# Kernel tuning notes

Measured on AMD Instinct MI355X. Metric: run time of the kernel, lower is better.

The kernel has to match this reference:

```python
import jax, jax.numpy as jnp
import numpy as np

B, LQ, LK, E, H = 4, 2048, 2048, 768, 12
D = E // H  # head_dim = 64
SCALE = 0.25 / np.sqrt(D)
LN_EPS = 1e-5


def _layernorm(x, g, b):
    mu = jnp.mean(x, axis=-1, keepdims=True)
    var = jnp.mean(jnp.square(x - mu), axis=-1, keepdims=True)
    return (x - mu) * jax.lax.rsqrt(var + LN_EPS) * g + b


def _rope(x, f):
    # x: [B,H,L,D]; f: [L,D//2,2] (real, imag) -- complex multiply on interleaved pairs
    xr = x.reshape(*x.shape[:-1], D // 2, 2)
    fr = f[None, None]  # [1,1,L,D//2,2]
    real = xr[..., 0] * fr[..., 0] - xr[..., 1] * fr[..., 1]
    imag = xr[..., 0] * fr[..., 1] + xr[..., 1] * fr[..., 0]
    return jnp.stack([real, imag], axis=-1).reshape(x.shape)


def setup_inputs() -> dict:
    key = jax.random.key(0)
    ks = jax.random.split(key, 8)
    x_q = jax.random.normal(ks[0], (B, LQ, E), jnp.float32)
    x_kv = jax.random.normal(ks[1], (B, LK, E), jnp.float32)
    # unit-magnitude rotary tables (cos, sin of random angles)
    ang_q = jax.random.uniform(ks[2], (LQ, D // 2), jnp.float32, 0.0, 2 * np.pi)
    ang_k = jax.random.uniform(ks[3], (LK, D // 2), jnp.float32, 0.0, 2 * np.pi)
    freqs_cis = jnp.stack([jnp.cos(ang_q), jnp.sin(ang_q)], axis=-1)
    freqs_cis_cross = jnp.stack([jnp.cos(ang_k), jnp.sin(ang_k)], axis=-1)
    Wq = jax.random.normal(ks[4], (E, E), jnp.float32) * 0.02
    Wkv = jax.random.normal(ks[5], (E, 2 * E), jnp.float32) * 0.02
    Wo = jax.random.normal(ks[6], (E, E), jnp.float32) * 0.02
    bo = jnp.zeros((E,), jnp.float32)
    return {
        'x_q': x_q, 'x_kv': x_kv,
        'freqs_cis': freqs_cis, 'freqs_cis_cross': freqs_cis_cross,
        'Wq': Wq, 'Wkv': Wkv, 'Wo': Wo, 'bo': bo,
        'ln_q_g': jnp.ones((E,), jnp.float32), 'ln_q_b': jnp.zeros((E,), jnp.float32),
        'ln_kv_g': jnp.ones((E,), jnp.float32), 'ln_kv_b': jnp.zeros((E,), jnp.float32),
        'gain': jnp.array(1.0, jnp.float32),
    }


def reference(x_q, x_kv, freqs_cis, freqs_cis_cross, Wq, Wkv, Wo, bo,
              ln_q_g, ln_q_b, ln_kv_g, ln_kv_b, gain):
    q = _layernorm(x_q, ln_q_g, ln_q_b) @ Wq                 # [B,LQ,E]
    kv = _layernorm(x_kv, ln_kv_g, ln_kv_b) @ Wkv            # [B,LK,2E]
    k, v = jnp.split(kv, 2, axis=-1)
    # b l (h d) -> b h l d
    q = q.reshape(B, LQ, H, D).transpose(0, 2, 1, 3)
    k = k.reshape(B, LK, H, D).transpose(0, 2, 1, 3)
    v = v.reshape(B, LK, H, D).transpose(0, 2, 1, 3)
    q = _rope(q, freqs_cis)
    k = _rope(k, freqs_cis_cross)
    attn = jnp.einsum('bhqd,bhkd->bhqk', q, k) * SCALE       # full O(L^2) matrix
    attn = jax.nn.softmax(attn, axis=-1)
    out = jnp.einsum('bhqk,bhkd->bhqd', attn, v)
    out = out.transpose(0, 2, 1, 3).reshape(B, LQ, E)        # b h l d -> b l (h d)
    return gain * (out @ Wo + bo)
```

## Files before the change

### kernel.cpp

```cpp
#include <hip/hip_runtime.h>
#include <hip/hip_bf16.h>

#define B_ 4
#define LQ_ 2048
#define LK_ 2048
#define E_ 768
#define H_ 12
#define D_ 64
#define SCALE_ 0.03125f
#define QSCALE_ 0.04508422f

using short8 = __attribute__((ext_vector_type(8))) short;
using f32x4  = __attribute__((ext_vector_type(4))) float;
using f32x16 = __attribute__((ext_vector_type(16))) float;

__device__ inline unsigned short f2bf(float f) {
    union { float f; unsigned u; } v; v.f = f;
    unsigned r = (v.u + 0x7FFFu + ((v.u >> 16) & 1u)) >> 16;
    return (unsigned short)r;
}

__device__ inline unsigned pkbf(float a, float b) {
    union { float f; unsigned u; } x, y; x.f = a; y.f = b;
    return ((x.u + 0x8000u) >> 16) | ((y.u + 0x8000u) & 0xffff0000u);
}

__device__ inline unsigned pkcvt(float a, float b) {
    float2 p; p.x = a; p.y = b;
    __hip_bfloat162 pb = __float22bfloat162_rn(p);
    union { __hip_bfloat162 h; unsigned u; } c; c.h = pb;
    return c.u;
}

__device__ inline void gll16(const void* g, void* l) {
    __builtin_amdgcn_global_load_lds(
        (const __attribute__((address_space(1))) unsigned int*)g,
        (__attribute__((address_space(3))) unsigned int*)l, 16, 0, 0);
}

__global__ __launch_bounds__(256) void ln_kernel(
    const float* __restrict__ xq, const float* __restrict__ xkv,
    const float* __restrict__ gq, const float* __restrict__ bq,
    const float* __restrict__ gk, const float* __restrict__ bk,
    unsigned short* __restrict__ yq, unsigned short* __restrict__ ykv)
{
    int wave = threadIdx.x >> 6, lane = threadIdx.x & 63;
    int row = blockIdx.x * 4 + wave;
    const float* x; const float* g; const float* be; unsigned short* y;
    if (row < 8192) { x = xq; g = gq; be = bq; y = yq; }
    else { row -= 8192; x = xkv; g = gk; be = bk; y = ykv; }
    const float* xr = x + (size_t)row * E_;
    float4 v[3];
    float s = 0.f;
#pragma unroll
    for (int i = 0; i < 3; i++) {
        v[i] = *(const float4*)(xr + i * 256 + lane * 4);
        s += v[i].x + v[i].y + v[i].z + v[i].w;
    }
#pragma unroll
    for (int off = 32; off >= 1; off >>= 1) s += __shfl_xor(s, off);
    float mu = s * (1.0f / E_);
    float q = 0.f;
#pragma unroll
    for (int i = 0; i < 3; i++) {
        float dx = v[i].x - mu, dy = v[i].y - mu, dz = v[i].z - mu, dw = v[i].w - mu;
        q += dx * dx + dy * dy + dz * dz + dw * dw;
    }
#pragma unroll
    for (int off = 32; off >= 1; off >>= 1) q += __shfl_xor(q, off);
    float rstd = rsqrtf(q * (1.0f / E_) + 1e-5f);
    unsigned short* yr = y + (size_t)row * E_;
#pragma unroll
    for (int i = 0; i < 3; i++) {
        int c = i * 256 + lane * 4;
        float4 gv = *(const float4*)(g + c);
        float4 bv = *(const float4*)(be + c);
        ushort4 o;
        o.x = f2bf((v[i].x - mu) * rstd * gv.x + bv.x);
        o.y = f2bf((v[i].y - mu) * rstd * gv.y + bv.y);
        o.z = f2bf((v[i].z - mu) * rstd * gv.z + bv.z);
        o.w = f2bf((v[i].w - mu) * rstd * gv.w + bv.w);
        *(ushort4*)(yr + c) = o;
    }
}

__global__ __launch_bounds__(256) void transpose3_kernel(
    const float* __restrict__ Wq, const float* __restrict__ Wkv, const float* __restrict__ Wo,
    unsigned short* __restrict__ WqT, unsigned short* __restrict__ WkvT, unsigned short* __restrict__ WoT)
{
    __shared__ float tile[32][33];
    int z = blockIdx.z;
    const float* in; unsigned short* out; int C;
    if (z == 0)      { in = Wq;  out = WqT;  C = E_; }
    else if (z == 1) { in = Wkv; out = WkvT; C = 2 * E_; }
    else             { in = Wo;  out = WoT;  C = E_; }
    int c0 = blockIdx.x * 32, r0 = blockIdx.y * 32;
    if (c0 >= C) return;
    int tx = threadIdx.x & 31, ty = threadIdx.x >> 5;
#pragma unroll
    for (int i = 0; i < 32; i += 8)
        tile[ty + i][tx] = in[(size_t)(r0 + ty + i) * C + c0 + tx];
    __syncthreads();
#pragma unroll
    for (int i = 0; i < 32; i += 8)
        out[(size_t)(c0 + ty + i) * E_ + r0 + tx] = f2bf(tile[tx][ty + i]);
}

#define BN 128
#define BK 64
template<int BMT>
__global__ __launch_bounds__(256) void gemm_kernel(
    const unsigned short* __restrict__ A, const unsigned short* __restrict__ Bt,
    int K, int mode,
    unsigned short* __restrict__ outQ, const float* __restrict__ freqs,
    unsigned short* __restrict__ outK, unsigned short* __restrict__ outV,
    float* __restrict__ outF, const float* __restrict__ bo, const float* __restrict__ gain)
{
    constexpr int MT = (BMT == 128) ? 4 : 2;
    constexpr int SMEMN = (BMT == 128) ? 128 * 136 : (BMT * 64 + 128 * 64);
    __shared__ __align__(16) unsigned short smem[SMEMN];
    auto Asm = (unsigned short (*)[BK])smem;
    auto Bsm = (unsigned short (*)[BK])(smem + BMT * BK);

    int tid = threadIdx.x;
    int wave = tid >> 6, lane = tid & 63;
    int quad = lane >> 4, l16 = lane & 15;
    int waveM = (wave >> 1) * (MT * 16), waveN = (wave & 1) * 64;
    int bm = blockIdx.x * BMT, bn = blockIdx.y * BN;
    int ro = lane >> 3, cx = lane & 7;
    int sco = ((cx ^ ro) * 8);

    f32x4 acc[MT][4] = {};

    for (int k0 = 0; k0 < K; k0 += BK) {
        const unsigned short* Ag = A + (size_t)(bm + wave * (BMT / 4) + ro) * K + k0 + sco;
        const unsigned short* Bg = Bt + (size_t)(bn + wave * 32 + ro) * K + k0 + sco;
#pragma unroll
        for (int i = 0; i < BMT / 32; i++)
            gll16(Ag + (size_t)(i * 8) * K, &Asm[wave * (BMT / 4) + i * 8][0]);
#pragma unroll
        for (int i = 0; i < 4; i++)
            gll16(Bg + (size_t)(i * 8) * K, &Bsm[wave * 32 + i * 8][0]);
        __syncthreads();
#pragma unroll
        for (int kk = 0; kk < BK; kk += 32) {
            short8 fa[MT], fb[4];
#pragma unroll
            for (int t = 0; t < 4; t++) {
                int pos = ((quad + (kk >> 3)) ^ (l16 & 7)) * 8;
                if (t < MT) fa[t] = *(const short8*)(&Asm[waveM + t * 16 + l16][pos]);
                fb[t] = *(const short8*)(&Bsm[waveN + t * 16 + l16][pos]);
            }
#pragma unroll
            for (int mt = 0; mt < MT; mt++)
#pragma unroll
                for (int nt = 0; nt < 4; nt++)
                    acc[mt][nt] = __builtin_amdgcn_mfma_f32_16x16x32_bf16(fa[mt], fb[nt], acc[mt][nt], 0, 0, 0);
        }
        __syncthreads();
    }

    if (BMT == 128 && mode == 1 && bn >= E_) {
        auto T = (unsigned short (*)[136])smem;
#pragma unroll
        for (int mt = 0; mt < MT; mt++) {
#pragma unroll
            for (int nt = 0; nt < 4; nt++) {
                int ml = waveM + mt * 16 + quad * 4;
                int nl = waveN + nt * 16 + l16;
                *(unsigned*)&T[nl][ml]     = pkbf(acc[mt][nt][0], acc[mt][nt][1]);
                *(unsigned*)&T[nl][ml + 2] = pkbf(acc[mt][nt][2], acc[mt][nt][3]);
            }
        }
        __syncthreads();
        int nnbase = bn - E_;
        int bb = bm >> 11, l0 = bm & (LQ_ - 1);
#pragma unroll
        for (int it = 0; it < 8; it++) {
            int row = it * 16 + (tid >> 4);
            int hh = (nnbase + row) >> 6, dd = (nnbase + row) & 63;
            short8 v = *(const short8*)&T[row][(tid & 15) * 8];
            *(short8*)(outV + (((size_t)bb * H_ + hh) * D_ + dd) * LK_ + l0 + (tid & 15) * 8) = v;
        }
        return;
    }

    float gg = (mode == 2) ? gain[0] : 0.f;
#pragma unroll
    for (int mt = 0; mt < MT; mt++) {
#pragma unroll
        for (int nt = 0; nt < 4; nt++) {
#pragma unroll
            for (int r = 0; r < 4; r++) {
                int m = bm + waveM + mt * 16 + quad * 4 + r;
                int n = bn + waveN + nt * 16 + l16;
                float v = acc[mt][nt][r];
                if (mode == 2) {
                    outF[(size_t)m * E_ + n] = gg * (v + bo[n]);
                } else {
                    int l = m & (LQ_ - 1), bb = m >> 11;
                    float partner = __shfl_xor(v, 1);
                    int h = n >> 6, dd = n & 63;
                    const float* f = freqs + ((size_t)l * 32 + (dd >> 1)) * 2;
                    float f0 = f[0], f1 = f[1];
                    float o = ((dd & 1) == 0) ? (v * f0 - partner * f1)
                                              : (partner * f1 + v * f0);
                    if (mode == 0) o *= QSCALE_;
                    unsigned short* dst = (mode == 0) ? outQ : outK;
                    dst[(((size_t)bb * H_ + h) * LQ_ + l) * D_ + dd] = f2bf(o);
                }
            }
        }
    }
}

__global__ __launch_bounds__(256) void attn_kernel(
    const unsigned short* __restrict__ Qg, const unsigned short* __restrict__ Kg,
    const unsigned short* __restrict__ Vt, unsigned short* __restrict__ O)
{
    __shared__ unsigned short Ksm[2][64][64];
    __shared__ unsigned short Vsm[2][64][64];

    int tid = threadIdx.x;
    int wave = tid >> 6, lane = tid & 63;
    int l32 = lane & 31, hi = lane >> 5;
    int bh = blockIdx.x;
    int b = bh / H_, h = bh % H_;
    int qbase = blockIdx.y * 128 + wave * 32;

    const size_t head = (size_t)bh * LK_ * D_;
    const unsigned short* Qh = Qg + head;
    const unsigned short* Kh = Kg + head;
    const unsigned short* Vh = Vt + head;

    short8 qf[4];
#pragma unroll
    for (int dc = 0; dc < 4; dc++)
        qf[dc] = *(const short8*)(Qh + (size_t)(qbase + l32) * D_ + dc * 16 + hi * 8);

    f32x16 oacc[2] = {};
    float lsum = 0.f;

    int ro = lane >> 3, cx = lane & 7;
    int sco = ((cx ^ ro) * 8);
    int sw = l32 & 7;

    {
        const unsigned short* Kp = Kh + (size_t)(wave * 16 + ro) * D_ + sco;
        const unsigned short* Vp = Vh + (size_t)(wave * 16 + ro) * LK_ + sco;
        gll16(Kp,            &Ksm[0][wave * 16][0]);
        gll16(Kp + 8 * D_,   &Ksm[0][wave * 16 + 8][0]);
        gll16(Vp,            &Vsm[0][wave * 16][0]);
        gll16(Vp + 8 * LK_,  &Vsm[0][wave * 16 + 8][0]);
    }
    asm volatile("s_waitcnt vmcnt(0)" ::: "memory");

    int buf = 0;
    for (int kt = 0; kt < LK_; kt += 64, buf ^= 1) {
        if (kt + 64 < LK_) {
            const unsigned short* Kp = Kh + (size_t)(kt + 64 + wave * 16 + ro) * D_ + sco;
            const unsigned short* Vp = Vh + (size_t)(wave * 16 + ro) * LK_ + kt + 64 + sco;
            gll16(Kp,           &Ksm[buf ^ 1][wave * 16][0]);
            gll16(Kp + 8 * D_,  &Ksm[buf ^ 1][wave * 16 + 8][0]);
            gll16(Vp,           &Vsm[buf ^ 1][wave * 16][0]);
            gll16(Vp + 8 * LK_, &Vsm[buf ^ 1][wave * 16 + 8][0]);
            asm volatile("s_waitcnt vmcnt(4)\ns_barrier" ::: "memory");
        } else {
            asm volatile("s_waitcnt vmcnt(0)\ns_barrier" ::: "memory");
        }

#pragma unroll
        for (int half = 0; half < 2; half++) {
            f32x16 st = {};
#pragma unroll
            for (int dc = 0; dc < 4; dc++) {
                int pos = ((dc * 2 + hi) ^ sw) * 8;
                short8 kfr = *(const short8*)(&Ksm[buf][half * 32 + l32][pos]);
                st = __builtin_amdgcn_mfma_f32_32x32x16_bf16(kfr, qf[dc], st, 0, 0, 0);
            }
            unsigned pks[8];
#pragma unroll
            for (int t = 0; t < 8; t++) {
                float p0 = __builtin_amdgcn_exp2f(st[2 * t]);
                float p1 = __builtin_amdgcn_exp2f(st[2 * t + 1]);
                lsum += p0 + p1;
                pks[t] = pkcvt(p0, p1);
            }
            unsigned y[8];
#pragma unroll
            for (int t = 0; t < 8; t++) y[t] = (unsigned)__shfl_xor((int)pks[t], 32);

#pragma unroll
            for (int kk = 0; kk < 2; kk++) {
                union { unsigned u[4]; short8 s; } pf;
#pragma unroll
                for (int g = 0; g < 4; g++) {
                    int t0 = kk * 4 + (g & 1);
                    unsigned own = hi ? pks[t0 + 2] : pks[t0];
                    unsigned oth = hi ? y[t0 + 2]   : y[t0];
                    pf.u[g] = ((g >> 1) == hi) ? own : oth;
                }
#pragma unroll
                for (int dt = 0; dt < 2; dt++) {
                    int pos = (((half * 2 + kk) * 2 + hi) ^ sw) * 8;
                    short8 vfr = *(const short8*)(&Vsm[buf][dt * 32 + l32][pos]);
                    oacc[dt] = __builtin_amdgcn_mfma_f32_32x32x16_bf16(pf.s, vfr, oacc[dt], 0, 0, 0);
                }
            }
        }
        asm volatile("s_waitcnt lgkmcnt(0)\ns_barrier" ::: "memory");
    }

    lsum += __shfl_xor(lsum, 32);
    float inv = 1.f / lsum;
#pragma unroll
    for (int reg = 0; reg < 16; reg++) {
        int ql = (reg & 3) + 8 * (reg >> 2) + 4 * hi;
        float iq = __shfl(inv, ql);
        int q = qbase + ql;
        size_t base = ((size_t)b * LQ_ + q) * E_ + h * D_;
#pragma unroll
        for (int dt = 0; dt < 2; dt++)
            O[base + dt * 32 + l32] = f2bf(oacc[dt][reg] * iq);
    }
}

extern "C" void kernel_launch(void* const* d_in, const int* in_sizes, int n_in,
                              void* d_out, int out_size, void* d_ws, size_t ws_size,
                              hipStream_t stream)
{
    const float* x_q     = (const float*)d_in[0];
    const float* x_kv    = (const float*)d_in[1];
    const float* freqs_q = (const float*)d_in[2];
    const float* freqs_k = (const float*)d_in[3];
    const float* Wq      = (const float*)d_in[4];
    const float* Wkv     = (const float*)d_in[5];
    const float* Wo      = (const float*)d_in[6];
    const float* bo      = (const float*)d_in[7];
    const float* ln_q_g  = (const float*)d_in[8];
    const float* ln_q_b  = (const float*)d_in[9];
    const float* ln_kv_g = (const float*)d_in[10];
    const float* ln_kv_b = (const float*)d_in[11];
    const float* gain    = (const float*)d_in[12];
    float* out = (float*)d_out;

    unsigned short* ws = (unsigned short*)d_ws;
    const size_t SZ = (size_t)B_ * LQ_ * E_;
    unsigned short* xq_ln  = ws;
    unsigned short* xkv_ln = xq_ln + SZ;
    unsigned short* Qb     = xkv_ln + SZ;
    unsigned short* Kb     = Qb + SZ;
    unsigned short* Vt     = Kb + SZ;
    unsigned short* Ob     = xq_ln;
    unsigned short* WqT    = Vt + SZ;
    unsigned short* WkvT   = WqT + E_ * E_;
    unsigned short* WoT    = WkvT + 2 * E_ * E_;

    ln_kernel<<<4096, 256, 0, stream>>>(x_q, x_kv, ln_q_g, ln_q_b, ln_kv_g, ln_kv_b,
                                        xq_ln, xkv_ln);
    transpose3_kernel<<<dim3(48, 24, 3), 256, 0, stream>>>(Wq, Wkv, Wo, WqT, WkvT, WoT);
    gemm_kernel<64><<<dim3(128, 6), 256, 0, stream>>>(xq_ln, WqT, E_, 0,
                                                      Qb, freqs_q, nullptr, nullptr, nullptr, nullptr, nullptr);
    gemm_kernel<128><<<dim3(64, 12), 256, 0, stream>>>(xkv_ln, WkvT, E_, 1,
                                                       nullptr, freqs_k, Kb, Vt, nullptr, nullptr, nullptr);
    attn_kernel<<<dim3(48, 16), 256, 0, stream>>>(Qb, Kb, Vt, Ob);
    gemm_kernel<64><<<dim3(128, 6), 256, 0, stream>>>(Ob, WoT, E_, 2,
                                                      nullptr, nullptr, nullptr, nullptr, out, bo, gain);
}
```

Baseline: 287.4 us.

## Split attention over two key halves, merge Q/KV GEMMs, drop P shuffles

Attention is split along the key dimension into two halves using a third grid dimension. Each half writes unnormalized partial outputs and row sums, and a new combine kernel adds them and normalizes. This doubles the number of attention blocks so the GPU is more fully occupied. The Q and KV projection GEMMs are fused into one launch with 128-row tiles. The per-iteration cross-lane shuffles of P are replaced by permuted V fragment loads from shared memory, and attn_kernel gets a minimum-occupancy launch bound. The cost is an extra pass over the partial outputs and extra rounding, since the partials are stored in bf16.

```diff
diff --git a/kernel.cpp b/kernel.cpp
--- a/kernel.cpp
+++ b/kernel.cpp
@@ -7,31 +7,31 @@
 #define E_ 768
 #define H_ 12
 #define D_ 64
-#define SCALE_ 0.03125f
 #define QSCALE_ 0.04508422f
 
 using short8 = __attribute__((ext_vector_type(8))) short;
 using f32x4  = __attribute__((ext_vector_type(4))) float;
 using f32x16 = __attribute__((ext_vector_type(16))) float;
+using uint2v = __attribute__((ext_vector_type(2))) unsigned;
 
 __device__ inline unsigned short f2bf(float f) {
     union { float f; unsigned u; } v; v.f = f;
     unsigned r = (v.u + 0x7FFFu + ((v.u >> 16) & 1u)) >> 16;
     return (unsigned short)r;
 }
-
+__device__ inline float bf2f(unsigned short u) {
+    union { unsigned u; float f; } v; v.u = ((unsigned)u) << 16; return v.f;
+}
 __device__ inline unsigned pkbf(float a, float b) {
     union { float f; unsigned u; } x, y; x.f = a; y.f = b;
     return ((x.u + 0x8000u) >> 16) | ((y.u + 0x8000u) & 0xffff0000u);
 }
-
 __device__ inline unsigned pkcvt(float a, float b) {
     float2 p; p.x = a; p.y = b;
     __hip_bfloat162 pb = __float22bfloat162_rn(p);
     union { __hip_bfloat162 h; unsigned u; } c; c.h = pb;
     return c.u;
 }
-
 __device__ inline void gll16(const void* g, void* l) {
     __builtin_amdgcn_global_load_lds(
         (const __attribute__((address_space(1))) unsigned int*)g,
@@ -106,53 +106,53 @@
         out[(size_t)(c0 + ty + i) * E_ + r0 + tx] = f2bf(tile[tx][ty + i]);
 }
 
-#define BN 128
 #define BK 64
-template<int BMT>
-__global__ __launch_bounds__(256) void gemm_kernel(
-    const unsigned short* __restrict__ A, const unsigned short* __restrict__ Bt,
-    int K, int mode,
-    unsigned short* __restrict__ outQ, const float* __restrict__ freqs,
-    unsigned short* __restrict__ outK, unsigned short* __restrict__ outV,
-    float* __restrict__ outF, const float* __restrict__ bo, const float* __restrict__ gain)
-{
-    constexpr int MT = (BMT == 128) ? 4 : 2;
-    constexpr int SMEMN = (BMT == 128) ? 128 * 136 : (BMT * 64 + 128 * 64);
-    __shared__ __align__(16) unsigned short smem[SMEMN];
+__global__ __launch_bounds__(256) void qkv_gemm(
+    const unsigned short* __restrict__ Aq, const unsigned short* __restrict__ Akv,
+    const unsigned short* __restrict__ WqT, const unsigned short* __restrict__ WkvT,
+    unsigned short* __restrict__ outQ, unsigned short* __restrict__ outK,
+    unsigned short* __restrict__ outV,
+    const float* __restrict__ freqs_q, const float* __restrict__ freqs_k)
+{
+    __shared__ __align__(16) unsigned short smem[128 * 136];
     auto Asm = (unsigned short (*)[BK])smem;
-    auto Bsm = (unsigned short (*)[BK])(smem + BMT * BK);
+    auto Bsm = (unsigned short (*)[BK])(smem + 128 * BK);
+
+    bool isQ = blockIdx.y < 6;
+    const unsigned short* A  = isQ ? Aq : Akv;
+    const unsigned short* Bt = isQ ? WqT : WkvT;
+    int bn = (isQ ? blockIdx.y : blockIdx.y - 6) * 128;
+    int bm = blockIdx.x * 128;
 
     int tid = threadIdx.x;
     int wave = tid >> 6, lane = tid & 63;
     int quad = lane >> 4, l16 = lane & 15;
-    int waveM = (wave >> 1) * (MT * 16), waveN = (wave & 1) * 64;
-    int bm = blockIdx.x * BMT, bn = blockIdx.y * BN;
+    int waveM = (wave >> 1) * 64, waveN = (wave & 1) * 64;
     int ro = lane >> 3, cx = lane & 7;
     int sco = ((cx ^ ro) * 8);
 
-    f32x4 acc[MT][4] = {};
-
-    for (int k0 = 0; k0 < K; k0 += BK) {
-        const unsigned short* Ag = A + (size_t)(bm + wave * (BMT / 4) + ro) * K + k0 + sco;
-        const unsigned short* Bg = Bt + (size_t)(bn + wave * 32 + ro) * K + k0 + sco;
-#pragma unroll
-        for (int i = 0; i < BMT / 32; i++)
-            gll16(Ag + (size_t)(i * 8) * K, &Asm[wave * (BMT / 4) + i * 8][0]);
-#pragma unroll
-        for (int i = 0; i < 4; i++)
-            gll16(Bg + (size_t)(i * 8) * K, &Bsm[wave * 32 + i * 8][0]);
+    f32x4 acc[4][4] = {};
+
+    for (int k0 = 0; k0 < E_; k0 += BK) {
+        const unsigned short* Ag = A + (size_t)(bm + wave * 32 + ro) * E_ + k0 + sco;
+        const unsigned short* Bg = Bt + (size_t)(bn + wave * 32 + ro) * E_ + k0 + sco;
+#pragma unroll
+        for (int i = 0; i < 4; i++) {
+            gll16(Ag + (size_t)(i * 8) * E_, &Asm[wave * 32 + i * 8][0]);
+            gll16(Bg + (size_t)(i * 8) * E_, &Bsm[wave * 32 + i * 8][0]);
+        }
         __syncthreads();
 #pragma unroll
         for (int kk = 0; kk < BK; kk += 32) {
-            short8 fa[MT], fb[4];
+            short8 fa[4], fb[4];
 #pragma unroll
             for (int t = 0; t < 4; t++) {
                 int pos = ((quad + (kk >> 3)) ^ (l16 & 7)) * 8;
-                if (t < MT) fa[t] = *(const short8*)(&Asm[waveM + t * 16 + l16][pos]);
+                fa[t] = *(const short8*)(&Asm[waveM + t * 16 + l16][pos]);
                 fb[t] = *(const short8*)(&Bsm[waveN + t * 16 + l16][pos]);
             }
 #pragma unroll
-            for (int mt = 0; mt < MT; mt++)
+            for (int mt = 0; mt < 4; mt++)
 #pragma unroll
                 for (int nt = 0; nt < 4; nt++)
                     acc[mt][nt] = __builtin_amdgcn_mfma_f32_16x16x32_bf16(fa[mt], fb[nt], acc[mt][nt], 0, 0, 0);
@@ -160,10 +160,10 @@
         __syncthreads();
     }
 
-    if (BMT == 128 && mode == 1 && bn >= E_) {
+    if (!isQ && bn >= E_) {
         auto T = (unsigned short (*)[136])smem;
 #pragma unroll
-        for (int mt = 0; mt < MT; mt++) {
+        for (int mt = 0; mt < 4; mt++) {
 #pragma unroll
             for (int nt = 0; nt < 4; nt++) {
                 int ml = waveM + mt * 16 + quad * 4;
@@ -185,9 +185,11 @@
         return;
     }
 
-    float gg = (mode == 2) ? gain[0] : 0.f;
-#pragma unroll
-    for (int mt = 0; mt < MT; mt++) {
+    float scl = isQ ? QSCALE_ : 1.0f;
+    const float* fr = isQ ? freqs_q : freqs_k;
+    unsigned short* dst = isQ ? outQ : outK;
+#pragma unroll
+    for (int mt = 0; mt < 4; mt++) {
 #pragma unroll
         for (int nt = 0; nt < 4; nt++) {
 #pragma unroll
@@ -195,28 +197,24 @@
                 int m = bm + waveM + mt * 16 + quad * 4 + r;
                 int n = bn + waveN + nt * 16 + l16;
                 float v = acc[mt][nt][r];
-                if (mode == 2) {
-                    outF[(size_t)m * E_ + n] = gg * (v + bo[n]);
-                } else {
-                    int l = m & (LQ_ - 1), bb = m >> 11;
-                    float partner = __shfl_xor(v, 1);
-                    int h = n >> 6, dd = n & 63;
-                    const float* f = freqs + ((size_t)l * 32 + (dd >> 1)) * 2;
-                    float f0 = f[0], f1 = f[1];
-                    float o = ((dd & 1) == 0) ? (v * f0 - partner * f1)
-                                              : (partner * f1 + v * f0);
-                    if (mode == 0) o *= QSCALE_;
-                    unsigned short* dst = (mode == 0) ? outQ : outK;
-                    dst[(((size_t)bb * H_ + h) * LQ_ + l) * D_ + dd] = f2bf(o);
-                }
-            }
-        }
-    }
-}
-
-__global__ __launch_bounds__(256) void attn_kernel(
+                int l = m & (LQ_ - 1), bb = m >> 11;
+                float partner = __shfl_xor(v, 1);
+                int h = n >> 6, dd = n & 63;
+                const float* f = fr + ((size_t)l * 32 + (dd >> 1)) * 2;
+                float f0 = f[0], f1 = f[1];
+                float o = ((dd & 1) == 0) ? (v * f0 - partner * f1)
+                                          : (partner * f1 + v * f0);
+                dst[(((size_t)bb * H_ + h) * LQ_ + l) * D_ + dd] = f2bf(o * scl);
+            }
+        }
+    }
+}
+
+__global__ __launch_bounds__(256, 5) void attn_kernel(
     const unsigned short* __restrict__ Qg, const unsigned short* __restrict__ Kg,
-    const unsigned short* __restrict__ Vt, unsigned short* __restrict__ O)
+    const unsigned short* __restrict__ Vt,
+    unsigned short* __restrict__ Op0, unsigned short* __restrict__ Op1,
+    float* __restrict__ Lp)
 {
     __shared__ unsigned short Ksm[2][64][64];
     __shared__ unsigned short Vsm[2][64][64];
@@ -225,12 +223,13 @@
     int wave = tid >> 6, lane = tid & 63;
     int l32 = lane & 31, hi = lane >> 5;
     int bh = blockIdx.x;
-    int b = bh / H_, h = bh % H_;
+    int z = blockIdx.z;
     int qbase = blockIdx.y * 128 + wave * 32;
+    int kt0 = z << 10;
 
     const size_t head = (size_t)bh * LK_ * D_;
     const unsigned short* Qh = Qg + head;
-    const unsigned short* Kh = Kg + head;
+    const unsigned short* Kh = Kg + head + (size_t)kt0 * D_;
     const unsigned short* Vh = Vt + head;
 
     short8 qf[4];
@@ -247,7 +246,7 @@
 
     {
         const unsigned short* Kp = Kh + (size_t)(wave * 16 + ro) * D_ + sco;
-        const unsigned short* Vp = Vh + (size_t)(wave * 16 + ro) * LK_ + sco;
+        const unsigned short* Vp = Vh + (size_t)(wave * 16 + ro) * LK_ + kt0 + sco;
         gll16(Kp,            &Ksm[0][wave * 16][0]);
         gll16(Kp + 8 * D_,   &Ksm[0][wave * 16 + 8][0]);
         gll16(Vp,            &Vsm[0][wave * 16][0]);
@@ -256,10 +255,11 @@
     asm volatile("s_waitcnt vmcnt(0)" ::: "memory");
 
     int buf = 0;
-    for (int kt = 0; kt < LK_; kt += 64, buf ^= 1) {
-        if (kt + 64 < LK_) {
-            const unsigned short* Kp = Kh + (size_t)(kt + 64 + wave * 16 + ro) * D_ + sco;
-            const unsigned short* Vp = Vh + (size_t)(wave * 16 + ro) * LK_ + kt + 64 + sco;
+    for (int it = 0; it < 16; it++, buf ^= 1) {
+        if (it < 15) {
+            int kn = (it + 1) * 64;
+            const unsigned short* Kp = Kh + (size_t)(kn + wave * 16 + ro) * D_ + sco;
+            const unsigned short* Vp = Vh + (size_t)(wave * 16 + ro) * LK_ + kt0 + kn + sco;
             gll16(Kp,           &Ksm[buf ^ 1][wave * 16][0]);
             gll16(Kp + 8 * D_,  &Ksm[buf ^ 1][wave * 16 + 8][0]);
             gll16(Vp,           &Vsm[buf ^ 1][wave * 16][0]);
@@ -286,43 +286,121 @@
                 lsum += p0 + p1;
                 pks[t] = pkcvt(p0, p1);
             }
-            unsigned y[8];
-#pragma unroll
-            for (int t = 0; t < 8; t++) y[t] = (unsigned)__shfl_xor((int)pks[t], 32);
-
 #pragma unroll
             for (int kk = 0; kk < 2; kk++) {
                 union { unsigned u[4]; short8 s; } pf;
-#pragma unroll
-                for (int g = 0; g < 4; g++) {
-                    int t0 = kk * 4 + (g & 1);
-                    unsigned own = hi ? pks[t0 + 2] : pks[t0];
-                    unsigned oth = hi ? y[t0 + 2]   : y[t0];
-                    pf.u[g] = ((g >> 1) == hi) ? own : oth;
+                pf.u[0] = pks[4 * kk + 0]; pf.u[1] = pks[4 * kk + 1];
+                pf.u[2] = pks[4 * kk + 2]; pf.u[3] = pks[4 * kk + 3];
+                int ch0 = half * 4 + kk * 2;
+#pragma unroll
+                for (int dt = 0; dt < 2; dt++) {
+                    int row = dt * 32 + l32;
+                    int e0 = ((ch0 ^ sw) * 8) + hi * 4;
+                    int e1 = (((ch0 + 1) ^ sw) * 8) + hi * 4;
+                    union { uint2v u2[2]; short8 s; } vf;
+                    vf.u2[0] = *(const uint2v*)(&Vsm[buf][row][e0]);
+                    vf.u2[1] = *(const uint2v*)(&Vsm[buf][row][e1]);
+                    oacc[dt] = __builtin_amdgcn_mfma_f32_32x32x16_bf16(pf.s, vf.s, oacc[dt], 0, 0, 0);
                 }
-#pragma unroll
-                for (int dt = 0; dt < 2; dt++) {
-                    int pos = (((half * 2 + kk) * 2 + hi) ^ sw) * 8;
-                    short8 vfr = *(const short8*)(&Vsm[buf][dt * 32 + l32][pos]);
-                    oacc[dt] = __builtin_amdgcn_mfma_f32_32x32x16_bf16(pf.s, vfr, oacc[dt], 0, 0, 0);
-                }
             }
         }
         asm volatile("s_waitcnt lgkmcnt(0)\ns_barrier" ::: "memory");
     }
 
     lsum += __shfl_xor(lsum, 32);
-    float inv = 1.f / lsum;
+    if (hi == 0)
+        Lp[((size_t)z * 48 + bh) * LQ_ + qbase + l32] = lsum;
+    unsigned short* Od = z ? Op1 : Op0;
 #pragma unroll
     for (int reg = 0; reg < 16; reg++) {
         int ql = (reg & 3) + 8 * (reg >> 2) + 4 * hi;
-        float iq = __shfl(inv, ql);
         int q = qbase + ql;
-        size_t base = ((size_t)b * LQ_ + q) * E_ + h * D_;
+        size_t base = ((size_t)bh * LQ_ + q) * D_;
 #pragma unroll
         for (int dt = 0; dt < 2; dt++)
-            O[base + dt * 32 + l32] = f2bf(oacc[dt][reg] * iq);
-    }
+            Od[base + dt * 32 + l32] = f2bf(oacc[dt][reg]);
+    }
+}
+
+__global__ __launch_bounds__(256) void combine_kernel(
+    const unsigned short* __restrict__ Op0, const unsigned short* __restrict__ Op1,
+    const float* __restrict__ Lp, unsigned short* __restrict__ Ob)
+{
+    const int PL = 48 * LQ_;
+    int t = blockIdx.x * 256 + threadIdx.x;
+    int chunk = t & 7;
+    int bhq = t >> 3;
+    size_t o = (size_t)bhq * D_ + chunk * 8;
+    short8 a = *(const short8*)(Op0 + o);
+    short8 b = *(const short8*)(Op1 + o);
+    float inv = 1.f / (Lp[bhq] + Lp[PL + bhq]);
+    int bh = bhq >> 11, q = bhq & (LQ_ - 1);
+    int bb = bh / H_, h = bh % H_;
+    short8 r;
+#pragma unroll
+    for (int j = 0; j < 8; j++) {
+        float s = bf2f((unsigned short)a[j]) + bf2f((unsigned short)b[j]);
+        r[j] = (short)f2bf(s * inv);
+    }
+    *(short8*)(Ob + ((size_t)(bb * LQ_ + q)) * E_ + h * D_ + chunk * 8) = r;
+}
+
+__global__ __launch_bounds__(256) void o_gemm(
+    const unsigned short* __restrict__ A, const unsigned short* __restrict__ Bt,
+    float* __restrict__ outF, const float* __restrict__ bo, const float* __restrict__ gain)
+{
+    __shared__ __align__(16) unsigned short smem[64 * BK + 128 * BK];
+    auto Asm = (unsigned short (*)[BK])smem;
+    auto Bsm = (unsigned short (*)[BK])(smem + 64 * BK);
+    int tid = threadIdx.x;
+    int wave = tid >> 6, lane = tid & 63;
+    int quad = lane >> 4, l16 = lane & 15;
+    int waveM = (wave >> 1) * 32, waveN = (wave & 1) * 64;
+    int bm = blockIdx.x * 64, bn = blockIdx.y * 128;
+    int ro = lane >> 3, cx = lane & 7;
+    int sco = ((cx ^ ro) * 8);
+
+    f32x4 acc[2][4] = {};
+
+    for (int k0 = 0; k0 < E_; k0 += BK) {
+        const unsigned short* Ag = A + (size_t)(bm + wave * 16 + ro) * E_ + k0 + sco;
+        const unsigned short* Bg = Bt + (size_t)(bn + wave * 32 + ro) * E_ + k0 + sco;
+#pragma unroll
+        for (int i = 0; i < 2; i++)
+            gll16(Ag + (size_t)(i * 8) * E_, &Asm[wave * 16 + i * 8][0]);
+#pragma unroll
+        for (int i = 0; i < 4; i++)
+            gll16(Bg + (size_t)(i * 8) * E_, &Bsm[wave * 32 + i * 8][0]);
+        __syncthreads();
+#pragma unroll
+        for (int kk = 0; kk < BK; kk += 32) {
+            short8 fa[2], fb[4];
+#pragma unroll
+            for (int t = 0; t < 4; t++) {
+                int pos = ((quad + (kk >> 3)) ^ (l16 & 7)) * 8;
+                if (t < 2) fa[t] = *(const short8*)(&Asm[waveM + t * 16 + l16][pos]);
+                fb[t] = *(const short8*)(&Bsm[waveN + t * 16 + l16][pos]);
+            }
+#pragma unroll
+            for (int mt = 0; mt < 2; mt++)
+#pragma unroll
+                for (int nt = 0; nt < 4; nt++)
+                    acc[mt][nt] = __builtin_amdgcn_mfma_f32_16x16x32_bf16(fa[mt], fb[nt], acc[mt][nt], 0, 0, 0);
+        }
+        __syncthreads();
+    }
+
+    float gg = gain[0];
+#pragma unroll
+    for (int mt = 0; mt < 2; mt++)
+#pragma unroll
+        for (int nt = 0; nt < 4; nt++)
+#pragma unroll
+            for (int r = 0; r < 4; r++) {
+                int m = bm + waveM + mt * 16 + quad * 4 + r;
+                int n = bn + waveN + nt * 16 + l16;
+                outF[(size_t)m * E_ + n] = gg * (acc[mt][nt][r] + bo[n]);
+            }
 }
 
 extern "C" void kernel_launch(void* const* d_in, const int* in_sizes, int n_in,
@@ -351,19 +429,20 @@
     unsigned short* Qb     = xkv_ln + SZ;
     unsigned short* Kb     = Qb + SZ;
     unsigned short* Vt     = Kb + SZ;
-    unsigned short* Ob     = xq_ln;
     unsigned short* WqT    = Vt + SZ;
     unsigned short* WkvT   = WqT + E_ * E_;
     unsigned short* WoT    = WkvT + 2 * E_ * E_;
+    unsigned short* Opz1   = WoT + E_ * E_;
+    float*          Lp     = (float*)(Opz1 + SZ);
+    unsigned short* Opz0   = xkv_ln;
+    unsigned short* Ob     = xq_ln;
 
     ln_kernel<<<4096, 256, 0, stream>>>(x_q, x_kv, ln_q_g, ln_q_b, ln_kv_g, ln_kv_b,
                                         xq_ln, xkv_ln);
     transpose3_kernel<<<dim3(48, 24, 3), 256, 0, stream>>>(Wq, Wkv, Wo, WqT, WkvT, WoT);
-    gemm_kernel<64><<<dim3(128, 6), 256, 0, stream>>>(xq_ln, WqT, E_, 0,
-                                                      Qb, freqs_q, nullptr, nullptr, nullptr, nullptr, nullptr);
-    gemm_kernel<128><<<dim3(64, 12), 256, 0, stream>>>(xkv_ln, WkvT, E_, 1,
-                                                       nullptr, freqs_k, Kb, Vt, nullptr, nullptr, nullptr);
-    attn_kernel<<<dim3(48, 16), 256, 0, stream>>>(Qb, Kb, Vt, Ob);
-    gemm_kernel<64><<<dim3(128, 6), 256, 0, stream>>>(Ob, WoT, E_, 2,
-                                                      nullptr, nullptr, nullptr, nullptr, out, bo, gain);
-}
+    qkv_gemm<<<dim3(64, 18), 256, 0, stream>>>(xq_ln, xkv_ln, WqT, WkvT,
+                                               Qb, Kb, Vt, freqs_q, freqs_k);
+    attn_kernel<<<dim3(48, 16, 2), 256, 0, stream>>>(Qb, Kb, Vt, Opz0, Opz1, Lp);
+    combine_kernel<<<3072, 256, 0, stream>>>(Opz0, Opz1, Lp, Ob);
+    o_gemm<<<dim3(128, 6), 256, 0, stream>>>(Ob, WoT, out, bo, gain);
+}
```

After: 294.8 us. +2.6%, slower.
